# Performance work log

Hardware: AMD Instinct MI355X
Metric: run time of the kernel (lower is better)

## Reference

```python
import jax, jax.numpy as jnp
import numpy as np

NODE_DIM = 128
NUM_IRREPS = 224          # 128 + 64 + 32 gates (one per irrep channel)
SPH_DIM = 480             # 128*1 + 64*3 + 32*5
HIDDEN = NODE_DIM + 2 * NUM_IRREPS  # 576
NUM_BASIS = 20
N_NODES = 10000
N_EDGES = 160000
# Each gate scalar is broadcast over its irrep's (2l+1) components.
_REPEATS = np.array([1] * 128 + [3] * 64 + [5] * 32)


def _expand_gate(g):
    # [E, 224] -> [E, 480], repeating each gate over its irrep dimension
    return jnp.repeat(g, _REPEATS, axis=-1, total_repeat_length=SPH_DIM)


def setup_inputs() -> dict:
    key = jax.random.key(0)
    ks = jax.random.split(key, 12)
    x_scalar = jax.random.normal(ks[0], (N_NODES, NODE_DIM), dtype=jnp.float32)
    x_spherical = jax.random.normal(ks[1], (N_NODES, SPH_DIM), dtype=jnp.float32)
    rbf = jax.random.uniform(ks[2], (N_EDGES, NUM_BASIS), dtype=jnp.float32)
    fcut = jax.random.uniform(ks[3], (N_EDGES, 1), dtype=jnp.float32)
    rsh = jax.random.normal(ks[4], (N_EDGES, SPH_DIM), dtype=jnp.float32)
    edge_index = jax.random.randint(ks[5], (2, N_EDGES), 0, N_NODES, dtype=jnp.int64)
    s1 = 1.0 / np.sqrt(NODE_DIM)
    s2 = 1.0 / np.sqrt(NUM_BASIS)
    W1 = jax.random.uniform(ks[6], (NODE_DIM, NODE_DIM), jnp.float32, -s1, s1)
    b1 = jnp.zeros((NODE_DIM,), jnp.float32)
    W2 = jax.random.uniform(ks[7], (NODE_DIM, HIDDEN), jnp.float32, -s1, s1)
    b2 = jnp.zeros((HIDDEN,), jnp.float32)
    Wr = jax.random.uniform(ks[8], (NUM_BASIS, HIDDEN), jnp.float32, -s2, s2)
    br = jnp.zeros((HIDDEN,), jnp.float32)
    return {"x_scalar": x_scalar, "x_spherical": x_spherical, "rbf": rbf,
            "fcut": fcut, "rsh": rsh, "edge_index": edge_index,
            "W1": W1, "b1": b1, "W2": W2, "b2": b2, "Wr": Wr, "br": br}


def reference(x_scalar, x_spherical, rbf, fcut, rsh, edge_index,
              W1, b1, W2, b2, Wr, br):
    src, dst = edge_index[0], edge_index[1]
    # scalar MLP: Linear -> SiLU -> Linear
    scalar_out = jax.nn.silu(x_scalar @ W1 + b1) @ W2 + b2          # [N, 576]
    filter_weight = (rbf @ Wr + br) * fcut                          # [E, 576]
    filter_out = scalar_out[dst] * filter_weight                    # [E, 576]
    gate_state = filter_out[:, :NUM_IRREPS]                         # [E, 224]
    gate_edge = filter_out[:, NUM_IRREPS:2 * NUM_IRREPS]            # [E, 224]
    message_scalar = filter_out[:, 2 * NUM_IRREPS:]                 # [E, 128]
    # ElementwiseTensorProduct(edge_irreps, '224x0e'): per-channel scalar gating
    message_spherical = (x_spherical[dst] * _expand_gate(gate_state)
                         + rsh * _expand_gate(gate_edge))           # [E, 480]
    new_scalar = x_scalar.at[src].add(message_scalar)
    new_spherical = x_spherical.at[src].add(message_spherical)
    return (new_scalar, new_spherical)
```

## Files before the change

kernel.cpp:

```cpp
#include <hip/hip_runtime.h>

#define NODE_DIM 128
#define NUM_IRREPS 224
#define SPH_DIM 480
#define HIDDEN 576
#define NUM_BASIS 20
#define N_NODES 10000
#define N_EDGES 160000
#define NPB 4
#define EB 16
#define NT 36
#define IRP (NUM_IRREPS + 8)

typedef __attribute__((ext_vector_type(8))) short short8v;
typedef __attribute__((ext_vector_type(4))) float f32x4;

__device__ __forceinline__ unsigned short f2bf(float f) {
    unsigned int u = __builtin_bit_cast(unsigned int, f);
    u = (u + 0x7fff + ((u >> 16) & 1)) >> 16;
    return (unsigned short)u;
}
__device__ __forceinline__ float bf2f(unsigned short h) {
    unsigned int u = ((unsigned int)h) << 16;
    return __builtin_bit_cast(float, u);
}

__global__ void init_out(const float* __restrict__ xs,
                         const float* __restrict__ xsp,
                         float* __restrict__ out,
                         int* __restrict__ counts) {
    const int stride = gridDim.x * blockDim.x;
    const int t0 = blockIdx.x * blockDim.x + threadIdx.x;
    for (int i = t0; i < N_NODES * NODE_DIM; i += stride) out[i] = xs[i];
    float* o2 = out + (size_t)N_NODES * NODE_DIM;
    for (int i = t0; i < N_NODES * SPH_DIM; i += stride) o2[i] = xsp[i];
    for (int i = t0; i < N_NODES; i += stride) counts[i] = 0;
}

__global__ __launch_bounds__(256) void hist_kernel(const int* __restrict__ eidx,
                                                   int* __restrict__ counts,
                                                   const float* __restrict__ Wr,
                                                   unsigned short* __restrict__ bfrag) {
    if (blockIdx.x == gridDim.x - 1) {
        for (int idx = threadIdx.x; idx < NT * 64; idx += 256) {
            const int nt = idx >> 6, l = idx & 63;
            const int col = nt * 16 + (l & 15);
            const int kb = (l >> 4) * 8;
            #pragma unroll
            for (int j = 0; j < 8; ++j) {
                const int k = kb + j;
                bfrag[(size_t)idx * 8 + j] = (k < NUM_BASIS) ? f2bf(Wr[k * HIDDEN + col]) : (unsigned short)0;
            }
        }
        return;
    }
    int i = blockIdx.x * blockDim.x + threadIdx.x;
    if (i < N_EDGES) atomicAdd(&counts[eidx[i]], 1);
}

__global__ __launch_bounds__(128) void node_mlp(
    const float* __restrict__ x,
    const float* __restrict__ W1, const float* __restrict__ b1,
    const float* __restrict__ W2, const float* __restrict__ b2,
    float* __restrict__ so) {
    __shared__ float xs[NPB][NODE_DIM];
    __shared__ float hs[NPB][NODE_DIM];
    const int tid = threadIdx.x;
    const int n0 = blockIdx.x * NPB;

    #pragma unroll
    for (int n = 0; n < NPB; ++n) {
        int node = n0 + n;
        xs[n][tid] = (node < N_NODES) ? x[(size_t)node * NODE_DIM + tid] : 0.f;
    }
    __syncthreads();

    float acc[NPB];
    #pragma unroll
    for (int n = 0; n < NPB; ++n) acc[n] = b1[tid];
    for (int k = 0; k < NODE_DIM; ++k) {
        float w = W1[k * NODE_DIM + tid];
        #pragma unroll
        for (int n = 0; n < NPB; ++n) acc[n] = fmaf(xs[n][k], w, acc[n]);
    }
    #pragma unroll
    for (int n = 0; n < NPB; ++n) {
        float v = acc[n];
        hs[n][tid] = v / (1.f + __expf(-v));
    }
    __syncthreads();

    for (int j = tid; j < HIDDEN; j += 128) {
        float a2[NPB];
        #pragma unroll
        for (int n = 0; n < NPB; ++n) a2[n] = b2[j];
        for (int k = 0; k < NODE_DIM; ++k) {
            float w = W2[k * HIDDEN + j];
            #pragma unroll
            for (int n = 0; n < NPB; ++n) a2[n] = fmaf(hs[n][k], w, a2[n]);
        }
        #pragma unroll
        for (int n = 0; n < NPB; ++n) {
            int node = n0 + n;
            if (node < N_NODES) so[(size_t)node * HIDDEN + j] = a2[n];
        }
    }
}

__global__ __launch_bounds__(1024) void scan_kernel(const int* __restrict__ counts,
                                                    int* __restrict__ offsets,
                                                    int* __restrict__ cursor) {
    __shared__ int wsum[16];
    const int tid = threadIdx.x;
    int vals[10];
    int run = 0;
    #pragma unroll
    for (int i = 0; i < 10; ++i) {
        int idx = tid * 10 + i;
        int c = (idx < N_NODES) ? counts[idx] : 0;
        vals[i] = run;
        run += c;
    }
    const int lane = tid & 63, w = tid >> 6;
    int inc = run;
    #pragma unroll
    for (int off = 1; off < 64; off <<= 1) {
        int v = __shfl_up(inc, off);
        if (lane >= off) inc += v;
    }
    if (lane == 63) wsum[w] = inc;
    __syncthreads();
    if (w == 0) {
        int v = (lane < 16) ? wsum[lane] : 0;
        #pragma unroll
        for (int off = 1; off < 16; off <<= 1) {
            int u = __shfl_up(v, off);
            if (lane >= off) v += u;
        }
        if (lane < 16) wsum[lane] = v;
    }
    __syncthreads();
    const int wbase = (w > 0) ? wsum[w - 1] : 0;
    const int base = wbase + inc - run;
    #pragma unroll
    for (int i = 0; i < 10; ++i) {
        int idx = tid * 10 + i;
        if (idx < N_NODES) {
            int v = base + vals[i];
            offsets[idx] = v;
            cursor[idx] = v;
        }
    }
    if (tid == 1023) offsets[N_NODES] = wbase + inc;
}

__global__ __launch_bounds__(256) void scatter_kernel(const int* __restrict__ eidx,
                                                      int* __restrict__ cursor,
                                                      int* __restrict__ edge_order,
                                                      int* __restrict__ edge_src) {
    int i = blockIdx.x * blockDim.x + threadIdx.x;
    if (i < N_EDGES) {
        int s = eidx[i];
        int pos = atomicAdd(&cursor[s], 1);
        edge_order[pos] = i;
        edge_src[pos] = s;
    }
}

__global__ __launch_bounds__(256, 8) void edge_mfma(
    const float* __restrict__ xsp,
    const float* __restrict__ rbf, const float* __restrict__ fcut,
    const float* __restrict__ rsh, const int* __restrict__ eidx,
    const unsigned short* __restrict__ bfrag, const float* __restrict__ br,
    const float* __restrict__ so,
    const int* __restrict__ edge_order, const int* __restrict__ edge_src,
    float* __restrict__ out_scalar, float* __restrict__ out_sph)
{
    __shared__ unsigned int   pair_s[EB][IRP];
    __shared__ unsigned short scal_s[EB][NODE_DIM + 8];
    __shared__ int   e_s[EB];
    __shared__ int   src_s[EB];
    __shared__ int   dst_s[EB];
    __shared__ float fc_s[EB];

    const int t = threadIdx.x;
    const int base = blockIdx.x * EB;
    const int lane = t & 63, w = t >> 6;

    const int m_row = lane & 15;
    const int kb = (lane >> 4) * 8;
    const int e_row = edge_order[base + m_row];
    short8v a0;
    {
        const float* rrow = rbf + (size_t)e_row * NUM_BASIS;
        #pragma unroll
        for (int j = 0; j < 8; ++j) {
            const int k = kb + j;
            a0[j] = (k < NUM_BASIS) ? (short)f2bf(rrow[k]) : (short)0;
        }
    }

    if (t < EB) {
        int pos = base + t;
        int e = edge_order[pos];
        e_s[t]   = e;
        src_s[t] = edge_src[pos];
        dst_s[t] = eidx[N_EDGES + e];
        fc_s[t]  = fcut[e];
    }
    __syncthreads();

    {
        const int rbase = (lane >> 4) * 4;
        int   dA[4];
        float fA[4];
        #pragma unroll
        for (int r = 0; r < 4; ++r) { dA[r] = dst_s[rbase + r]; fA[r] = fc_s[rbase + r]; }
        #pragma unroll
        for (int i = 0; i < NT / 4; ++i) {
            const int nt = w * (NT / 4) + i;
            const short8v bf = *(const short8v*)(bfrag + (size_t)(nt * 64 + lane) * 8);
            f32x4 c0 = {0.f, 0.f, 0.f, 0.f};
            c0 = __builtin_amdgcn_mfma_f32_16x16x32_bf16(a0, bf, c0, 0, 0, 0);
            const int col = nt * 16 + (lane & 15);
            const float brc = br[col];
            #pragma unroll
            for (int r = 0; r < 4; ++r) {
                const int row = rbase + r;
                const float v = (c0[r] + brc) * fA[r] * so[(size_t)dA[r] * HIDDEN + col];
                const unsigned short hv = f2bf(v);
                if (col < NUM_IRREPS) {
                    ((unsigned short*)&pair_s[row][col])[0] = hv;
                } else if (col < 2 * NUM_IRREPS) {
                    ((unsigned short*)&pair_s[row][col - NUM_IRREPS])[1] = hv;
                } else {
                    scal_s[row][col - 2 * NUM_IRREPS] = hv;
                }
            }
        }
    }
    __syncthreads();

    const int g1i = (t < 128) ? t : (128 + (t - 128) / 3);
    const int g2i = (t < 64) ? (128 + (128 + t) / 3) : (192 + (t - 64) / 5);

    float accS = 0.f, accD1 = 0.f, accD2 = 0.f;
    int cur_src = src_s[0];

    #pragma unroll 4
    for (int le = 0; le < EB; ++le) {
        const int s = src_s[le];
        if (s != cur_src) {
            atomicAdd(&out_sph[(size_t)cur_src * SPH_DIM + t], accD1);
            if (t < 224) atomicAdd(&out_sph[(size_t)cur_src * SPH_DIM + 256 + t], accD2);
            if (t < 128) atomicAdd(&out_scalar[(size_t)cur_src * NODE_DIM + t], accS);
            accD1 = accD2 = accS = 0.f;
            cur_src = s;
        }
        const int dst = dst_s[le];
        const int eg  = e_s[le];
        const float xv1 = xsp[(size_t)dst * SPH_DIM + t];
        const float rv1 = rsh[(size_t)eg  * SPH_DIM + t];
        const unsigned int p1 = pair_s[le][g1i];
        accD1 = fmaf(xv1, bf2f((unsigned short)(p1 & 0xffffu)),
                fmaf(rv1, bf2f((unsigned short)(p1 >> 16)), accD1));
        if (t < 224) {
            const float xv2 = xsp[(size_t)dst * SPH_DIM + 256 + t];
            const float rv2 = rsh[(size_t)eg  * SPH_DIM + 256 + t];
            const unsigned int p2 = pair_s[le][g2i];
            accD2 = fmaf(xv2, bf2f((unsigned short)(p2 & 0xffffu)),
                    fmaf(rv2, bf2f((unsigned short)(p2 >> 16)), accD2));
        }
        if (t < 128) accS += bf2f(scal_s[le][t]);
    }
    atomicAdd(&out_sph[(size_t)cur_src * SPH_DIM + t], accD1);
    if (t < 224) atomicAdd(&out_sph[(size_t)cur_src * SPH_DIM + 256 + t], accD2);
    if (t < 128) atomicAdd(&out_scalar[(size_t)cur_src * NODE_DIM + t], accS);
}

extern "C" void kernel_launch(void* const* d_in, const int* in_sizes, int n_in,
                              void* d_out, int out_size, void* d_ws, size_t ws_size,
                              hipStream_t stream) {
    const float* x_scalar    = (const float*)d_in[0];
    const float* x_spherical = (const float*)d_in[1];
    const float* rbf         = (const float*)d_in[2];
    const float* fcut        = (const float*)d_in[3];
    const float* rsh         = (const float*)d_in[4];
    const int*   eidx        = (const int*)d_in[5];
    const float* W1          = (const float*)d_in[6];
    const float* b1          = (const float*)d_in[7];
    const float* W2          = (const float*)d_in[8];
    const float* b2          = (const float*)d_in[9];
    const float* Wr          = (const float*)d_in[10];
    const float* br          = (const float*)d_in[11];

    float* out        = (float*)d_out;
    float* out_scalar = out;
    float* out_sph    = out + (size_t)N_NODES * NODE_DIM;

    float* scalar_out = (float*)d_ws;
    int*   counts     = (int*)(scalar_out + (size_t)N_NODES * HIDDEN);
    int*   offsets    = counts + N_NODES;
    int*   cursor     = offsets + N_NODES + 1;
    int*   edge_order = cursor + N_NODES;
    int*   edge_src   = edge_order + N_EDGES;
    unsigned short* bfrag = (unsigned short*)((((uintptr_t)(edge_src + N_EDGES)) + 15) & ~(uintptr_t)15);

    init_out<<<2048, 256, 0, stream>>>(x_scalar, x_spherical, out, counts);
    hist_kernel<<<N_EDGES / 256 + 1, 256, 0, stream>>>(eidx, counts, Wr, bfrag);
    scan_kernel<<<1, 1024, 0, stream>>>(counts, offsets, cursor);
    scatter_kernel<<<(N_EDGES + 255) / 256, 256, 0, stream>>>(eidx, cursor, edge_order, edge_src);
    node_mlp<<<(N_NODES + NPB - 1) / NPB, 128, 0, stream>>>(x_scalar, W1, b1, W2, b2, scalar_out);
    edge_mfma<<<N_EDGES / EB, 256, 0, stream>>>(x_spherical, rbf, fcut, rsh, eidx,
                                                bfrag, br, scalar_out, edge_order, edge_src,
                                                out_scalar, out_sph);
}
```

Baseline: 319.5 us.

## Prefetch edge gather rows into registers before MFMA and fuse prep kernels

Before the MFMA filter computation, edge_mfma now loads all 16 edges' x_spherical and rsh values into register arrays, so the gather latency overlaps the MFMA work instead of being serialized in the accumulation loop. The occupancy hint drops from 8 to 4 waves to leave room for the extra registers. The LDS row paddings change to odd strides to reduce bank conflicts. init_out and hist_kernel are merged into one prep kernel, with the counts zeroed by a memset, which removes a launch at the cost of lower occupancy and higher register pressure.

After: 394.7 us. +23.5%, slower.

```diff
diff --git a/kernel.cpp b/kernel.cpp
--- a/kernel.cpp
+++ b/kernel.cpp
@@ -10,7 +10,8 @@
 #define NPB 4
 #define EB 16
 #define NT 36
-#define IRP (NUM_IRREPS + 8)
+#define IRP 233
+#define SCP 138
 
 typedef __attribute__((ext_vector_type(8))) short short8v;
 typedef __attribute__((ext_vector_type(4))) float f32x4;
@@ -25,22 +26,17 @@
     return __builtin_bit_cast(float, u);
 }
 
-__global__ void init_out(const float* __restrict__ xs,
-                         const float* __restrict__ xsp,
-                         float* __restrict__ out,
-                         int* __restrict__ counts) {
+__global__ __launch_bounds__(256) void prep_kernel(
+    const float* __restrict__ xs, const float* __restrict__ xsp,
+    float* __restrict__ out,
+    const int* __restrict__ eidx, int* __restrict__ counts,
+    const float* __restrict__ Wr, unsigned short* __restrict__ bfrag) {
     const int stride = gridDim.x * blockDim.x;
-    const int t0 = blockIdx.x * blockDim.x + threadIdx.x;
-    for (int i = t0; i < N_NODES * NODE_DIM; i += stride) out[i] = xs[i];
+    const int gt = blockIdx.x * blockDim.x + threadIdx.x;
+    for (int i = gt; i < N_NODES * NODE_DIM; i += stride) out[i] = xs[i];
     float* o2 = out + (size_t)N_NODES * NODE_DIM;
-    for (int i = t0; i < N_NODES * SPH_DIM; i += stride) o2[i] = xsp[i];
-    for (int i = t0; i < N_NODES; i += stride) counts[i] = 0;
-}
-
-__global__ __launch_bounds__(256) void hist_kernel(const int* __restrict__ eidx,
-                                                   int* __restrict__ counts,
-                                                   const float* __restrict__ Wr,
-                                                   unsigned short* __restrict__ bfrag) {
+    for (int i = gt; i < N_NODES * SPH_DIM; i += stride) o2[i] = xsp[i];
+    if (gt < N_EDGES) atomicAdd(&counts[eidx[gt]], 1);
     if (blockIdx.x == gridDim.x - 1) {
         for (int idx = threadIdx.x; idx < NT * 64; idx += 256) {
             const int nt = idx >> 6, l = idx & 63;
@@ -52,10 +48,7 @@
                 bfrag[(size_t)idx * 8 + j] = (k < NUM_BASIS) ? f2bf(Wr[k * HIDDEN + col]) : (unsigned short)0;
             }
         }
-        return;
-    }
-    int i = blockIdx.x * blockDim.x + threadIdx.x;
-    if (i < N_EDGES) atomicAdd(&counts[eidx[i]], 1);
+    }
 }
 
 __global__ __launch_bounds__(128) void node_mlp(
@@ -167,7 +160,7 @@
     }
 }
 
-__global__ __launch_bounds__(256, 8) void edge_mfma(
+__global__ __launch_bounds__(256, 4) void edge_mfma(
     const float* __restrict__ xsp,
     const float* __restrict__ rbf, const float* __restrict__ fcut,
     const float* __restrict__ rsh, const int* __restrict__ eidx,
@@ -177,7 +170,7 @@
     float* __restrict__ out_scalar, float* __restrict__ out_sph)
 {
     __shared__ unsigned int   pair_s[EB][IRP];
-    __shared__ unsigned short scal_s[EB][NODE_DIM + 8];
+    __shared__ unsigned short scal_s[EB][SCP];
     __shared__ int   e_s[EB];
     __shared__ int   src_s[EB];
     __shared__ int   dst_s[EB];
@@ -209,6 +202,19 @@
         fc_s[t]  = fcut[e];
     }
     __syncthreads();
+
+    float xv1[EB], rv1[EB], xv2[EB], rv2[EB];
+    #pragma unroll
+    for (int le = 0; le < EB; ++le) {
+        const int dst = dst_s[le];
+        const int eg  = e_s[le];
+        const float* xr = xsp + (size_t)dst * SPH_DIM;
+        const float* rr = rsh + (size_t)eg  * SPH_DIM;
+        xv1[le] = xr[t];
+        rv1[le] = rr[t];
+        if (t < 224) { xv2[le] = xr[256 + t]; rv2[le] = rr[256 + t]; }
+        else         { xv2[le] = 0.f;         rv2[le] = 0.f; }
+    }
 
     {
         const int rbase = (lane >> 4) * 4;
@@ -247,7 +253,7 @@
     float accS = 0.f, accD1 = 0.f, accD2 = 0.f;
     int cur_src = src_s[0];
 
-    #pragma unroll 4
+    #pragma unroll
     for (int le = 0; le < EB; ++le) {
         const int s = src_s[le];
         if (s != cur_src) {
@@ -257,19 +263,13 @@
             accD1 = accD2 = accS = 0.f;
             cur_src = s;
         }
-        const int dst = dst_s[le];
-        const int eg  = e_s[le];
-        const float xv1 = xsp[(size_t)dst * SPH_DIM + t];
-        const float rv1 = rsh[(size_t)eg  * SPH_DIM + t];
         const unsigned int p1 = pair_s[le][g1i];
-        accD1 = fmaf(xv1, bf2f((unsigned short)(p1 & 0xffffu)),
-                fmaf(rv1, bf2f((unsigned short)(p1 >> 16)), accD1));
+        accD1 = fmaf(xv1[le], bf2f((unsigned short)(p1 & 0xffffu)),
+                fmaf(rv1[le], bf2f((unsigned short)(p1 >> 16)), accD1));
         if (t < 224) {
-            const float xv2 = xsp[(size_t)dst * SPH_DIM + 256 + t];
-            const float rv2 = rsh[(size_t)eg  * SPH_DIM + 256 + t];
             const unsigned int p2 = pair_s[le][g2i];
-            accD2 = fmaf(xv2, bf2f((unsigned short)(p2 & 0xffffu)),
-                    fmaf(rv2, bf2f((unsigned short)(p2 >> 16)), accD2));
+            accD2 = fmaf(xv2[le], bf2f((unsigned short)(p2 & 0xffffu)),
+                    fmaf(rv2[le], bf2f((unsigned short)(p2 >> 16)), accD2));
         }
         if (t < 128) accS += bf2f(scal_s[le][t]);
     }
@@ -306,8 +306,8 @@
     int*   edge_src   = edge_order + N_EDGES;
     unsigned short* bfrag = (unsigned short*)((((uintptr_t)(edge_src + N_EDGES)) + 15) & ~(uintptr_t)15);
 
-    init_out<<<2048, 256, 0, stream>>>(x_scalar, x_spherical, out, counts);
-    hist_kernel<<<N_EDGES / 256 + 1, 256, 0, stream>>>(eidx, counts, Wr, bfrag);
+    hipMemsetAsync(counts, 0, N_NODES * sizeof(int), stream);
+    prep_kernel<<<2048, 256, 0, stream>>>(x_scalar, x_spherical, out, eidx, counts, Wr, bfrag);
     scan_kernel<<<1, 1024, 0, stream>>>(counts, offsets, cursor);
     scatter_kernel<<<(N_EDGES + 255) / 256, 256, 0, stream>>>(eidx, cursor, edge_order, edge_src);
     node_mlp<<<(N_NODES + NPB - 1) / NPB, 128, 0, stream>>>(x_scalar, W1, b1, W2, b2, scalar_out);
```
